# Kernel tuning notes

Measured on AMD Instinct MI355X. Metric: run time of the kernel, lower is better.

## Reference

```python
import jax, jax.numpy as jnp
import numpy as np

N_NODES = 50000
N_EDGES = 800000
IN_CH, HID, OUT_CH = 128, 256, 40


def setup_inputs() -> dict:
    key = jax.random.key(0)
    ks = jax.random.split(key, 10)
    x = jax.random.normal(ks[0], (N_NODES, IN_CH), dtype=jnp.float32)
    edge_index = jax.random.randint(ks[1], (2, N_EDGES), 0, N_NODES, dtype=jnp.int64)
    s = 0.05  # weight init scale
    return {
        "x": x,
        "edge_index": edge_index,
        "W1a": jax.random.normal(ks[2], (IN_CH, HID), dtype=jnp.float32) * s,
        "b1a": jnp.zeros((HID,), jnp.float32),
        "W2a": jax.random.normal(ks[3], (HID, HID), dtype=jnp.float32) * s,
        "b2a": jnp.zeros((HID,), jnp.float32),
        "W1b": jax.random.normal(ks[4], (HID, HID), dtype=jnp.float32) * s,
        "b1b": jnp.zeros((HID,), jnp.float32),
        "W2b": jax.random.normal(ks[5], (HID, HID), dtype=jnp.float32) * s,
        "b2b": jnp.zeros((HID,), jnp.float32),
        "Wlin": jax.random.normal(ks[6], (HID * 2, OUT_CH), dtype=jnp.float32) * s,
        "blin": jnp.zeros((OUT_CH,), jnp.float32),
    }


def _gin_conv(h, src, dst, W1, b1, W2, b2):
    # sum-aggregate messages h[src] into destination nodes, eps = 0
    agg = jax.ops.segment_sum(h[src], dst, num_segments=N_NODES)
    z = h + agg
    z = jnp.maximum(z @ W1 + b1, 0.0) @ W2 + b2  # 2-layer MLP
    return z


def reference(x, edge_index, W1a, b1a, W2a, b2a, W1b, b1b, W2b, b2b, Wlin, blin):
    src, dst = edge_index[0], edge_index[1]
    h1 = jnp.maximum(_gin_conv(x, src, dst, W1a, b1a, W2a, b2a), 0.0)
    h2 = jnp.maximum(_gin_conv(h1, src, dst, W1b, b1b, W2b, b2b), 0.0)
    h_cat = jnp.concatenate([h1, h2], axis=1)  # [N, 2*HID]
    logits = h_cat @ Wlin + blin
    return jax.nn.log_softmax(logits, axis=1)
```

## Files before the change

### kernel.cpp

```cpp
#include <hip/hip_runtime.h>
#include <math.h>

#define N_NODES 50000
#define N_EDGES 800000
#define IN_CH 128
#define HID 256
#define OUT_CH 40
#define GRP 6250
#define HGRP 3125
#define NCHUNK 32
#define TS 264

typedef unsigned short u16;
typedef unsigned char u8;
typedef __attribute__((ext_vector_type(8))) short bf16x8;
typedef __attribute__((ext_vector_type(8))) unsigned short u16x8;
typedef __attribute__((ext_vector_type(4))) float f32x4;
typedef __attribute__((ext_vector_type(2))) float f32x2;

__device__ __forceinline__ float bf2f(u16 u) {
    union { unsigned int i; float f; } v; v.i = ((unsigned int)u) << 16; return v.f;
}
__device__ __forceinline__ u16 f2bf(float f) {
    union { float f; unsigned int i; } v; v.f = f;
    unsigned int x = v.i;
    x += 0x7fffu + ((x >> 16) & 1u);
    return (u16)(x >> 16);
}

#define GLOBAL_AS __attribute__((address_space(1)))
#define LDS_AS __attribute__((address_space(3)))
__device__ __forceinline__ void async_cp16(const void* g, void* l) {
    __builtin_amdgcn_global_load_lds((const GLOBAL_AS unsigned int*)g,
                                     (LDS_AS unsigned int*)l, 16, 0, 0);
}

__device__ __forceinline__ void pack_w(
    const float* __restrict__ in, u16* __restrict__ out, int K, int N, int c)
{
    for (int k = threadIdx.x; k < K; k += 256) {
        int kk32 = k >> 5, quad = (k >> 3) & 3, e = k & 7;
        size_t base = (((size_t)c * (K >> 5) + kk32) * 64 + quad * 16) * 8 + e;
#pragma unroll
        for (int li = 0; li < 16; li++) {
            int n = c * 16 + li;
            float v = (n < N) ? in[(size_t)k * N + n] : 0.f;
            out[base + (size_t)li * 8] = f2bf(v);
        }
    }
}

__global__ __launch_bounds__(256) void prep_fused(
    const float* __restrict__ x, u16* __restrict__ xb, u8* __restrict__ xf8,
    const int* __restrict__ ei, u16* __restrict__ e16,
    const float* __restrict__ W1a, const float* __restrict__ W2a,
    const float* __restrict__ W1b, const float* __restrict__ W2b,
    const float* __restrict__ Wlin,
    u16* __restrict__ W1aPk, u16* __restrict__ W2aPk,
    u16* __restrict__ W1bPk, u16* __restrict__ W2bPk, u16* __restrict__ WlinPk,
    u16* __restrict__ partial)
{
    __shared__ int hist[HGRP];
    int b = blockIdx.x;
    if (b < 6250) {
        int i = b * 256 + threadIdx.x;
        float4 v = ((const float4*)x)[i];
        ushort4 o;
        o.x = f2bf(v.x); o.y = f2bf(v.y); o.z = f2bf(v.z); o.w = f2bf(v.w);
        ((ushort4*)xb)[i] = o;
        int p = __builtin_amdgcn_cvt_pk_fp8_f32(v.x, v.y, 0, false);
        p = __builtin_amdgcn_cvt_pk_fp8_f32(v.z, v.w, p, true);
        ((unsigned int*)xf8)[i] = (unsigned int)p;
    } else if (b < 7813) {
        int i = (b - 6250) * 256 + threadIdx.x;
        if (i < (2 * N_EDGES) / 4) {
            int4 v = ((const int4*)ei)[i];
            ushort4 o;
            o.x = (u16)v.x; o.y = (u16)v.y; o.z = (u16)v.z; o.w = (u16)v.w;
            ((ushort4*)e16)[i] = o;
        }
    } else if (b < 7880) {
        int t = b - 7813;
        if (t < 16)       pack_w(W1a, W1aPk, IN_CH, HID, t);
        else if (t < 32)  pack_w(W2a, W2aPk, HID, HID, t - 16);
        else if (t < 48)  pack_w(W1b, W1bPk, HID, HID, t - 32);
        else if (t < 64)  pack_w(W2b, W2bPk, HID, HID, t - 48);
        else              pack_w(Wlin, WlinPk, 2 * HID, OUT_CH, t - 64);
    } else {
        const int hb = b - 7880;
        const int gh = hb & 15;
        const int sub = hb >> 4;
        const int lo = gh * HGRP;
        const int CH = N_EDGES / NCHUNK;
        for (int i = threadIdx.x; i < HGRP; i += 256) hist[i] = 0;
        __syncthreads();
        const int4* dsts = (const int4*)(ei + N_EDGES + sub * CH);
        for (int k = threadIdx.x; k < CH / 4; k += 256) {
            int4 d = dsts[k];
            int r0 = d.x - lo, r1 = d.y - lo;
            int r2 = d.z - lo, r3 = d.w - lo;
            if ((unsigned)r0 < (unsigned)HGRP) atomicAdd(&hist[r0], 1);
            if ((unsigned)r1 < (unsigned)HGRP) atomicAdd(&hist[r1], 1);
            if ((unsigned)r2 < (unsigned)HGRP) atomicAdd(&hist[r2], 1);
            if ((unsigned)r3 < (unsigned)HGRP) atomicAdd(&hist[r3], 1);
        }
        __syncthreads();
        u16* po = partial + (size_t)(sub * 8 + (gh >> 1)) * GRP + (gh & 1) * HGRP;
        for (int i = threadIdx.x; i < HGRP; i += 256) po[i] = (u16)hist[i];
    }
}

__global__ __launch_bounds__(256) void scan1(
    const u16* __restrict__ partial, u16* __restrict__ chunkpref,
    int* __restrict__ excl, int* __restrict__ partials_out)
{
    __shared__ int lds[256];
    const int tid = threadIdx.x;
    const int node = blockIdx.x * 256 + tid;
    int d = 0;
    if (node < N_NODES) {
        int g = node / GRP;
        int off = node - g * GRP;
#pragma unroll
        for (int sub = 0; sub < NCHUNK; sub++) {
            chunkpref[(size_t)sub * N_NODES + node] = (u16)d;
            d += partial[(size_t)(sub * 8 + g) * GRP + off];
        }
    }
    lds[tid] = d;
    __syncthreads();
    for (int off = 1; off < 256; off <<= 1) {
        int t = (tid >= off) ? lds[tid - off] : 0;
        __syncthreads();
        lds[tid] += t;
        __syncthreads();
    }
    if (node < N_NODES) excl[node] = lds[tid] - d;
    if (tid == 255) partials_out[blockIdx.x] = lds[255];
}

__global__ __launch_bounds__(256) void scan3(
    int* __restrict__ excl, const int* __restrict__ partials,
    int* __restrict__ sentinel, int nPart)
{
    __shared__ int lds[256];
    __shared__ int bp[256];
    const int tid = threadIdx.x;
    int orig = (tid < nPart) ? partials[tid] : 0;
    lds[tid] = orig;
    __syncthreads();
    for (int off = 1; off < 256; off <<= 1) {
        int t = (tid >= off) ? lds[tid - off] : 0;
        __syncthreads();
        lds[tid] += t;
        __syncthreads();
    }
    bp[tid] = lds[tid] - orig;
    __syncthreads();
    const int idx = blockIdx.x * 256 + tid;
    if (idx < N_NODES) excl[idx] += bp[blockIdx.x];
    if (idx == 0) sentinel[0] = N_EDGES;
}

__global__ __launch_bounds__(256) void csr_fill(
    const u16* __restrict__ src16, const u16* __restrict__ dst16,
    const int* __restrict__ rowp, const u16* __restrict__ chunkpref,
    u16* __restrict__ csr_src)
{
    __shared__ int cur[HGRP];
    const int gh = blockIdx.x & 15;
    const int c = blockIdx.x >> 4;
    const int lo = gh * HGRP;
    const int CH = N_EDGES / NCHUNK;
    const u16* cp = chunkpref + (size_t)c * N_NODES + lo;
    for (int i = threadIdx.x; i < HGRP; i += 256)
        cur[i] = rowp[lo + i] + cp[i];
    __syncthreads();
    const ushort4* dsts = (const ushort4*)(dst16 + c * CH);
    const ushort4* srcs = (const ushort4*)(src16 + c * CH);
    for (int k = threadIdx.x; k < CH / 4; k += 256) {
        ushort4 d = dsts[k];
        ushort4 sc = srcs[k];
        int r0 = (int)d.x - lo, r1 = (int)d.y - lo;
        int r2 = (int)d.z - lo, r3 = (int)d.w - lo;
        if ((unsigned)r0 < (unsigned)HGRP) { int p = atomicAdd(&cur[r0], 1); csr_src[p] = sc.x; }
        if ((unsigned)r1 < (unsigned)HGRP) { int p = atomicAdd(&cur[r1], 1); csr_src[p] = sc.y; }
        if ((unsigned)r2 < (unsigned)HGRP) { int p = atomicAdd(&cur[r2], 1); csr_src[p] = sc.z; }
        if ((unsigned)r3 < (unsigned)HGRP) { int p = atomicAdd(&cur[r3], 1); csr_src[p] = sc.w; }
    }
}


__global__ __launch_bounds__(256) void gather_agg_f8_128(
    const u16* __restrict__ feat_bf, const u8* __restrict__ feat_f8,
    const int* __restrict__ row_ptr, const int* __restrict__ row_end,
    const u16* __restrict__ csr_src, u16* __restrict__ out)
{
    const int tid = threadIdx.x;
    const int lane = tid & 63;
    const int wv = tid >> 6;
    const int li = lane & 7;
    int node = blockIdx.x * 32 + wv * 8 + (lane >> 3);
    const bool valid = node < N_NODES;
    if (!valid) node = N_NODES - 1;

    int j = row_ptr[node];
    int deg = valid ? (row_end[node] - j) : 0;

    float acc[16];
    {
        u16x8 s0 = *(const u16x8*)(feat_bf + (size_t)node * IN_CH + li * 16);
        u16x8 s1 = *(const u16x8*)(feat_bf + (size_t)node * IN_CH + li * 16 + 8);
#pragma unroll
        for (int q = 0; q < 8; q++) { acc[q] = bf2f(s0[q]); acc[8 + q] = bf2f(s1[q]); }
    }

    int maxdeg = deg;
#pragma unroll
    for (int off = 8; off < 64; off <<= 1)
        maxdeg = max(maxdeg, __shfl_xor(maxdeg, off, 64));

    for (int it = 0; it < maxdeg; it += 4) {
        int4 g0 = {0,0,0,0}, g1 = {0,0,0,0}, g2 = {0,0,0,0}, g3 = {0,0,0,0};
        if (it < deg)
            g0 = *(const int4*)(feat_f8 + (size_t)csr_src[j + it] * IN_CH + li * 16);
        if (it + 1 < deg)
            g1 = *(const int4*)(feat_f8 + (size_t)csr_src[j + it + 1] * IN_CH + li * 16);
        if (it + 2 < deg)
            g2 = *(const int4*)(feat_f8 + (size_t)csr_src[j + it + 2] * IN_CH + li * 16);
        if (it + 3 < deg)
            g3 = *(const int4*)(feat_f8 + (size_t)csr_src[j + it + 3] * IN_CH + li * 16);
#pragma unroll
        for (int q = 0; q < 4; q++) {
            int w0 = (&g0.x)[q], w1 = (&g1.x)[q], w2 = (&g2.x)[q], w3 = (&g3.x)[q];
            f32x2 l0 = __builtin_amdgcn_cvt_pk_f32_fp8(w0, false);
            f32x2 h0 = __builtin_amdgcn_cvt_pk_f32_fp8(w0, true);
            f32x2 l1 = __builtin_amdgcn_cvt_pk_f32_fp8(w1, false);
            f32x2 h1 = __builtin_amdgcn_cvt_pk_f32_fp8(w1, true);
            f32x2 l2 = __builtin_amdgcn_cvt_pk_f32_fp8(w2, false);
            f32x2 h2 = __builtin_amdgcn_cvt_pk_f32_fp8(w2, true);
            f32x2 l3 = __builtin_amdgcn_cvt_pk_f32_fp8(w3, false);
            f32x2 h3 = __builtin_amdgcn_cvt_pk_f32_fp8(w3, true);
            acc[q * 4 + 0] += (l0.x + l1.x) + (l2.x + l3.x);
            acc[q * 4 + 1] += (l0.y + l1.y) + (l2.y + l3.y);
            acc[q * 4 + 2] += (h0.x + h1.x) + (h2.x + h3.x);
            acc[q * 4 + 3] += (h0.y + h1.y) + (h2.y + h3.y);
        }
    }

    if (valid) {
        u16x8 o0, o1;
#pragma unroll
        for (int q = 0; q < 8; q++) { o0[q] = f2bf(acc[q]); o1[q] = f2bf(acc[8 + q]); }
        *(u16x8*)(out + (size_t)node * IN_CH + li * 16) = o0;
        *(u16x8*)(out + (size_t)node * IN_CH + li * 16 + 8) = o1;
    }
}

__global__ __launch_bounds__(256) void gather_agg_f8_256(
    const u16* __restrict__ feat_bf, const u8* __restrict__ feat_f8,
    const int* __restrict__ row_ptr, const int* __restrict__ row_end,
    const u16* __restrict__ csr_src, u16* __restrict__ out)
{
    const int tid = threadIdx.x;
    const int lane = tid & 63;
    const int wv = tid >> 6;
    const int li = lane & 15;
    const int node = blockIdx.x * 16 + wv * 4 + (lane >> 4);

    int j = row_ptr[node];
    int deg = row_end[node] - j;

    float acc[16];
    {
        u16x8 s0 = *(const u16x8*)(feat_bf + (size_t)node * HID + li * 16);
        u16x8 s1 = *(const u16x8*)(feat_bf + (size_t)node * HID + li * 16 + 8);
#pragma unroll
        for (int q = 0; q < 8; q++) { acc[q] = bf2f(s0[q]); acc[8 + q] = bf2f(s1[q]); }
    }

    int maxdeg = deg;
#pragma unroll
    for (int off = 16; off < 64; off <<= 1)
        maxdeg = max(maxdeg, __shfl_xor(maxdeg, off, 64));

    for (int it = 0; it < maxdeg; it += 4) {
        int4 g0 = {0,0,0,0}, g1 = {0,0,0,0}, g2 = {0,0,0,0}, g3 = {0,0,0,0};
        if (it < deg)
            g0 = *(const int4*)(feat_f8 + (size_t)csr_src[j + it] * HID + li * 16);
        if (it + 1 < deg)
            g1 = *(const int4*)(feat_f8 + (size_t)csr_src[j + it + 1] * HID + li * 16);
        if (it + 2 < deg)
            g2 = *(const int4*)(feat_f8 + (size_t)csr_src[j + it + 2] * HID + li * 16);
        if (it + 3 < deg)
            g3 = *(const int4*)(feat_f8 + (size_t)csr_src[j + it + 3] * HID + li * 16);
#pragma unroll
        for (int q = 0; q < 4; q++) {
            int w0 = (&g0.x)[q], w1 = (&g1.x)[q], w2 = (&g2.x)[q], w3 = (&g3.x)[q];
            f32x2 l0 = __builtin_amdgcn_cvt_pk_f32_fp8(w0, false);
            f32x2 h0 = __builtin_amdgcn_cvt_pk_f32_fp8(w0, true);
            f32x2 l1 = __builtin_amdgcn_cvt_pk_f32_fp8(w1, false);
            f32x2 h1 = __builtin_amdgcn_cvt_pk_f32_fp8(w1, true);
            f32x2 l2 = __builtin_amdgcn_cvt_pk_f32_fp8(w2, false);
            f32x2 h2 = __builtin_amdgcn_cvt_pk_f32_fp8(w2, true);
            f32x2 l3 = __builtin_amdgcn_cvt_pk_f32_fp8(w3, false);
            f32x2 h3 = __builtin_amdgcn_cvt_pk_f32_fp8(w3, true);
            acc[q * 4 + 0] += (l0.x + l1.x) + (l2.x + l3.x);
            acc[q * 4 + 1] += (l0.y + l1.y) + (l2.y + l3.y);
            acc[q * 4 + 2] += (h0.x + h1.x) + (h2.x + h3.x);
            acc[q * 4 + 3] += (h0.y + h1.y) + (h2.y + h3.y);
        }
    }

    u16x8 o0, o1;
#pragma unroll
    for (int q = 0; q < 8; q++) { o0[q] = f2bf(acc[q]); o1[q] = f2bf(acc[8 + q]); }
    *(u16x8*)(out + (size_t)node * HID + li * 16) = o0;
    *(u16x8*)(out + (size_t)node * HID + li * 16 + 8) = o1;
}

__global__ __launch_bounds__(256, 4) void mlp_fused(
    const u16* __restrict__ A, int K1,
    const u16* __restrict__ W1pk, const float* __restrict__ b1,
    const u16* __restrict__ W2pk, const float* __restrict__ b2,
    u16* __restrict__ out, u8* __restrict__ outF8, int M)
{
    __shared__ u16 SB[64 * TS];

    const int tid = threadIdx.x;
    const int lane = tid & 63;
    const int wid = tid >> 6;
    const int li = lane & 15;
    const int quad = lane >> 4;
    const int koff = quad * 8;
    const int row0 = blockIdx.x * 64;
    const int KB1 = K1 >> 5;
    const int rsh = (K1 == 256) ? 9 : 8;

    {
        const u8* Ag = (const u8*)(A + (size_t)row0 * K1);
        const int rounds = K1 >> 5;
        for (int j = 0; j < rounds; j++) {
            int L = (j * 256 + tid) * 16;
            int G = L ^ (((L >> rsh) & 7) << 4);
            async_cp16(Ag + G, (u8*)SB + L);
        }
    }

    f32x4 acc[4][4];
#pragma unroll
    for (int i = 0; i < 4; i++)
#pragma unroll
        for (int j = 0; j < 4; j++) acc[i][j] = (f32x4){0.f, 0.f, 0.f, 0.f};

#define LDW(WF, WPK, KB, KK32)                                                \
    {   _Pragma("unroll")                                                     \
        for (int t = 0; t < 4; t++)                                           \
            WF[t] = *(const bf16x8*)((WPK) +                                  \
                (((size_t)(wid * 4 + t) * (KB) + (KK32)) * 64 + lane) * 8); }
#define LDA1(AF, KK)                                                          \
    {   _Pragma("unroll")                                                     \
        for (int t = 0; t < 4; t++) {                                         \
            int row = t * 16 + li;                                            \
            int bo = row * (K1 * 2) + ((KK) + koff) * 2;                      \
            bo ^= (row & 7) << 4;                                             \
            AF[t] = *(const bf16x8*)((const u8*)SB + bo); } }
#define LDA2(AF, KK)                                                          \
    {   _Pragma("unroll")                                                     \
        for (int t = 0; t < 4; t++)                                           \
            AF[t] = *(const bf16x8*)(SB + (t * 16 + li) * TS + (KK) + koff); }
#define MFMA16(AF, WF)                                                        \
    {   _Pragma("unroll")                                                     \
        for (int mt = 0; mt < 4; mt++)                                        \
            _Pragma("unroll")                                                 \
            for (int nt = 0; nt < 4; nt++)                                    \
                acc[mt][nt] = __builtin_amdgcn_mfma_f32_16x16x32_bf16(        \
                    AF[mt], WF[nt], acc[mt][nt], 0, 0, 0); }

    bf16x8 wfA[4], wfB[4], af[4];

    LDW(wfA, W1pk, KB1, 0);
    __syncthreads();

    for (int kk32 = 0; kk32 < KB1; kk32 += 2) {
        LDW(wfB, W1pk, KB1, kk32 + 1);
        LDA1(af, kk32 * 32);
        MFMA16(af, wfA);
        if (kk32 + 2 < KB1) LDW(wfA, W1pk, KB1, kk32 + 2);
        LDA1(af, kk32 * 32 + 32);
        MFMA16(af, wfB);
    }
    __syncthreads();

#pragma unroll
    for (int nt = 0; nt < 4; nt++) {
        int col = wid * 64 + nt * 16 + li;
        float bv = b1[col];
#pragma unroll
        for (int mt = 0; mt < 4; mt++) {
#pragma unroll
            for (int reg = 0; reg < 4; reg++) {
                int row = mt * 16 + quad * 4 + reg;
                float v = fmaxf(acc[mt][nt][reg] + bv, 0.f);
                SB[row * TS + col] = f2bf(v);
                acc[mt][nt][reg] = 0.f;
            }
        }
    }
    LDW(wfA, W2pk, 8, 0);
    __syncthreads();

    for (int kk32 = 0; kk32 < 8; kk32 += 2) {
        LDW(wfB, W2pk, 8, kk32 + 1);
        LDA2(af, kk32 * 32);
        MFMA16(af, wfA);
        if (kk32 + 2 < 8) LDW(wfA, W2pk, 8, kk32 + 2);
        LDA2(af, kk32 * 32 + 32);
        MFMA16(af, wfB);
    }
#undef LDW
#undef LDA1
#undef LDA2
#undef MFMA16

    __syncthreads();
#pragma unroll
    for (int nt = 0; nt < 4; nt++) {
        int col = wid * 64 + nt * 16 + li;
        float bv = b2[col];
#pragma unroll
        for (int mt = 0; mt < 4; mt++) {
#pragma unroll
            for (int reg = 0; reg < 4; reg++) {
                int row = mt * 16 + quad * 4 + reg;
                float v = fmaxf(acc[mt][nt][reg] + bv, 0.f);
                SB[row * TS + col] = f2bf(v);
            }
        }
    }
    __syncthreads();
#pragma unroll
    for (int it = 0; it < 8; it++) {
        int flat = it * 4096 + tid * 16;
        int r = flat >> 9;
        int cu = (flat & 511) >> 1;
        int row = row0 + r;
        if (row < M) {
            u16x8 v = *(const u16x8*)(SB + r * TS + cu);
            *(u16x8*)(out + (size_t)row * HID + cu) = v;
            if (outF8 != nullptr) {
                int p0 = __builtin_amdgcn_cvt_pk_fp8_f32(bf2f(v[0]), bf2f(v[1]), 0, false);
                p0 = __builtin_amdgcn_cvt_pk_fp8_f32(bf2f(v[2]), bf2f(v[3]), p0, true);
                int p1 = __builtin_amdgcn_cvt_pk_fp8_f32(bf2f(v[4]), bf2f(v[5]), 0, false);
                p1 = __builtin_amdgcn_cvt_pk_fp8_f32(bf2f(v[6]), bf2f(v[7]), p1, true);
                int2 pv; pv.x = p0; pv.y = p1;
                *(int2*)(outF8 + (size_t)row * HID + cu) = pv;
            }
        }
    }
}

__global__ __launch_bounds__(256, 6) void gemm_mfma(
    const u16* __restrict__ A, const u16* __restrict__ Acat, int Ksplit, int ldA,
    const u16* __restrict__ Bpk, const float* __restrict__ bias,
    float* __restrict__ out, int M, int K)
{
    const int tid = threadIdx.x;
    const int lane = tid & 63;
    const int wid = tid >> 6;
    const int li = lane & 15;
    const int quad = lane >> 4;
    const int koff = quad * 8;
    const int row0 = blockIdx.x * 64 + wid * 16;

    f32x4 acc[3];
#pragma unroll
    for (int i = 0; i < 3; i++) acc[i] = (f32x4){0.f, 0.f, 0.f, 0.f};

    int r = row0 + li;
    const int arow = (r < M) ? r : (M - 1);
    const int KB = K >> 5;

#define LD_G(AF, BF, KK)                                                      \
    {   const u16* Ab = ((KK) >= Ksplit) ? Acat : A;                          \
        const int kb = ((KK) >= Ksplit) ? ((KK) - Ksplit) : (KK);             \
        AF = *(const bf16x8*)(Ab + (size_t)arow * ldA + kb + koff);           \
        _Pragma("unroll")                                                     \
        for (int t = 0; t < 3; t++)                                           \
            BF[t] = *(const bf16x8*)(Bpk +                                    \
                (((size_t)t * KB + ((KK) >> 5)) * 64 + lane) * 8); }
#define MFMA3(AF, BF)                                                         \
    {   _Pragma("unroll")                                                     \
        for (int nt = 0; nt < 3; nt++)                                        \
            acc[nt] = __builtin_amdgcn_mfma_f32_16x16x32_bf16(                \
                AF, BF[nt], acc[nt], 0, 0, 0); }

    {
        bf16x8 a0, b0[3], a1, b1v[3];
        LD_G(a0, b0, 0);
        for (int kk = 0; kk < K; kk += 64) {
            LD_G(a1, b1v, kk + 32);
            MFMA3(a0, b0);
            if (kk + 64 < K) LD_G(a0, b0, kk + 64);
            MFMA3(a1, b1v);
        }
    }
#undef LD_G
#undef MFMA3

    float b0v = bias[li];
    float b1s = bias[16 + li];
    float b2s = (li < 8) ? bias[32 + li] : 0.f;
#pragma unroll
    for (int reg = 0; reg < 4; reg++) {
        int row = row0 + quad * 4 + reg;
        float v0 = acc[0][reg] + b0v;
        float v1 = acc[1][reg] + b1s;
        float v2 = (li < 8) ? (acc[2][reg] + b2s) : -INFINITY;
        float m = fmaxf(fmaxf(v0, v1), v2);
#pragma unroll
        for (int off = 1; off < 16; off <<= 1)
            m = fmaxf(m, __shfl_xor(m, off, 64));
        float s = expf(v0 - m) + expf(v1 - m)
                + ((li < 8) ? expf(v2 - m) : 0.f);
#pragma unroll
        for (int off = 1; off < 16; off <<= 1)
            s += __shfl_xor(s, off, 64);
        float lg = m + logf(s);
        if (row < M) {
            out[(size_t)row * OUT_CH + li] = v0 - lg;
            out[(size_t)row * OUT_CH + 16 + li] = v1 - lg;
            if (li < 8) out[(size_t)row * OUT_CH + 32 + li] = v2 - lg;
        }
    }
}

extern "C" void kernel_launch(void* const* d_in, const int* in_sizes, int n_in,
                              void* d_out, int out_size, void* d_ws, size_t ws_size,
                              hipStream_t stream)
{
    const float* x    = (const float*)d_in[0];
    const int*   ei   = (const int*)d_in[1];
    const float* W1a  = (const float*)d_in[2];
    const float* b1a  = (const float*)d_in[3];
    const float* W2a  = (const float*)d_in[4];
    const float* b2a  = (const float*)d_in[5];
    const float* W1b  = (const float*)d_in[6];
    const float* b1b  = (const float*)d_in[7];
    const float* W2b  = (const float*)d_in[8];
    const float* b2b  = (const float*)d_in[9];
    const float* Wlin = (const float*)d_in[10];
    const float* blin = (const float*)d_in[11];
    float* out = (float*)d_out;

    const size_t R = (size_t)N_NODES * HID;
    u16* R0 = (u16*)d_ws;
    u16* R1 = R0 + R;
    u16* R2 = R1 + R;
    u16* R3 = R2 + R;
    u16* R4 = R3 + R;
    u16* xbf = R0;
    u16* zA  = R1;
    u16* partial = (u16*)R1;
    u8*  xf8 = (u8*)(R1 + (size_t)N_NODES * IN_CH);
    u8*  h1f8 = (u8*)R1;
    u16* h1  = R3;
    u16* zB  = R4;
    u16* h2  = R2;

    u16* wts = R4 + R;
    u16* W1aPk = wts;
    u16* W2aPk = W1aPk + 256 * 128;
    u16* W1bPk = W2aPk + 256 * 256;
    u16* W2bPk = W1bPk + 256 * 256;
    u16* WlinPk = W2bPk + 256 * 256;
    int* rowp   = (int*)(WlinPk + 128 * 512);
    int* part   = rowp + N_NODES + 64;
    u16* csr    = (u16*)(part + 256);
    u16* e16    = csr + N_EDGES;
    u16* src16  = e16;
    u16* dst16  = e16 + N_EDGES;
    u16* chunkpref = dst16 + N_EDGES;

    dim3 blk(256);
    const int scanBlocks = (N_NODES + 255) / 256;
    const int agg128Blocks = (N_NODES + 31) / 32;
    const int agg256Blocks = N_NODES / 16;
    const int mlpBlocks  = (N_NODES + 63) / 64;
    const int gemmBlocks = (N_NODES + 63) / 64;

    prep_fused<<<8392, blk, 0, stream>>>(x, xbf, xf8, ei, e16,
                                         W1a, W2a, W1b, W2b, Wlin,
                                         W1aPk, W2aPk, W1bPk, W2bPk, WlinPk,
                                         partial);
    scan1<<<scanBlocks, blk, 0, stream>>>(partial, chunkpref, rowp, part);
    scan3<<<scanBlocks, blk, 0, stream>>>(rowp, part, rowp + N_NODES, scanBlocks);
    csr_fill<<<16 * NCHUNK, blk, 0, stream>>>(src16, dst16, rowp, chunkpref, csr);

    gather_agg_f8_128<<<agg128Blocks, blk, 0, stream>>>(xbf, xf8, rowp, rowp + 1, csr, zA);
    mlp_fused<<<mlpBlocks, blk, 0, stream>>>(zA, IN_CH, W1aPk, b1a, W2aPk, b2a,
                                             h1, h1f8, N_NODES);

    gather_agg_f8_256<<<agg256Blocks, blk, 0, stream>>>(h1, h1f8, rowp, rowp + 1, csr, zB);
    mlp_fused<<<mlpBlocks, blk, 0, stream>>>(zB, HID, W1bPk, b1b, W2bPk, b2b,
                                             h2, nullptr, N_NODES);

    gemm_mfma<<<gemmBlocks, blk, 0, stream>>>(h1, h2, HID, HID, WlinPk, blin,
                                              out, N_NODES, 2 * HID);
}
```

Baseline: 252.1 us.

## Swizzle MLP shared tile and stage final GEMM A rows through LDS

The fused MLP kernel drops its padded shared-memory row stride (264) for an unpadded 256-wide tile with an XOR swizzle. This shrinks LDS per block so occupancy can rise from 4 to 5 blocks. The final linear+log_softmax GEMM now copies each 64-row tile of h1 and then h2 into a swizzled LDS buffer with async copies before running the MFMAs, where it previously loaded A fragments straight from global memory. The goal is coalesced global reads; the cost is extra LDS usage, extra barriers and occupancy lowered from 6 to 5 in the GEMM. The GEMM tail no longer clamps rows past M, so the last block may read past the end of h1/h2.

```diff
diff --git a/kernel.cpp b/kernel.cpp
--- a/kernel.cpp
+++ b/kernel.cpp
@@ -9,7 +9,6 @@
 #define GRP 6250
 #define HGRP 3125
 #define NCHUNK 32
-#define TS 264
 
 typedef unsigned short u16;
 typedef unsigned char u8;
@@ -319,13 +318,13 @@
     *(u16x8*)(out + (size_t)node * HID + li * 16 + 8) = o1;
 }
 
-__global__ __launch_bounds__(256, 4) void mlp_fused(
+__global__ __launch_bounds__(256, 5) void mlp_fused(
     const u16* __restrict__ A, int K1,
     const u16* __restrict__ W1pk, const float* __restrict__ b1,
     const u16* __restrict__ W2pk, const float* __restrict__ b2,
     u16* __restrict__ out, u8* __restrict__ outF8, int M)
 {
-    __shared__ u16 SB[64 * TS];
+    __shared__ u16 SB[64 * 256];
 
     const int tid = threadIdx.x;
     const int lane = tid & 63;
@@ -367,8 +366,10 @@
             AF[t] = *(const bf16x8*)((const u8*)SB + bo); } }
 #define LDA2(AF, KK)                                                          \
     {   _Pragma("unroll")                                                     \
-        for (int t = 0; t < 4; t++)                                           \
-            AF[t] = *(const bf16x8*)(SB + (t * 16 + li) * TS + (KK) + koff); }
+        for (int t = 0; t < 4; t++) {                                         \
+            int row = t * 16 + li;                                            \
+            int ix = (row * 256 + (KK) + koff) ^ ((row & 7) << 3);            \
+            AF[t] = *(const bf16x8*)(SB + ix); } }
 #define MFMA16(AF, WF)                                                        \
     {   _Pragma("unroll")                                                     \
         for (int mt = 0; mt < 4; mt++)                                        \
@@ -402,7 +403,7 @@
             for (int reg = 0; reg < 4; reg++) {
                 int row = mt * 16 + quad * 4 + reg;
                 float v = fmaxf(acc[mt][nt][reg] + bv, 0.f);
-                SB[row * TS + col] = f2bf(v);
+                SB[(row * 256 + col) ^ ((row & 7) << 3)] = f2bf(v);
                 acc[mt][nt][reg] = 0.f;
             }
         }
@@ -434,7 +435,7 @@
             for (int reg = 0; reg < 4; reg++) {
                 int row = mt * 16 + quad * 4 + reg;
                 float v = fmaxf(acc[mt][nt][reg] + bv, 0.f);
-                SB[row * TS + col] = f2bf(v);
+                SB[(row * 256 + col) ^ ((row & 7) << 3)] = f2bf(v);
             }
         }
     }
@@ -446,7 +447,8 @@
         int cu = (flat & 511) >> 1;
         int row = row0 + r;
         if (row < M) {
-            u16x8 v = *(const u16x8*)(SB + r * TS + cu);
+            int ix = (r * 256 + cu) ^ ((r & 7) << 3);
+            u16x8 v = *(const u16x8*)(SB + ix);
             *(u16x8*)(out + (size_t)row * HID + cu) = v;
             if (outF8 != nullptr) {
                 int p0 = __builtin_amdgcn_cvt_pk_fp8_f32(bf2f(v[0]), bf2f(v[1]), 0, false);
@@ -460,52 +462,76 @@
     }
 }
 
-__global__ __launch_bounds__(256, 6) void gemm_mfma(
-    const u16* __restrict__ A, const u16* __restrict__ Acat, int Ksplit, int ldA,
+__global__ __launch_bounds__(256, 5) void gemm_mfma(
+    const u16* __restrict__ A, const u16* __restrict__ Acat,
     const u16* __restrict__ Bpk, const float* __restrict__ bias,
-    float* __restrict__ out, int M, int K)
-{
+    float* __restrict__ out, int M)
+{
+    __shared__ u16 SA[64 * 256];
+
     const int tid = threadIdx.x;
     const int lane = tid & 63;
     const int wid = tid >> 6;
     const int li = lane & 15;
     const int quad = lane >> 4;
     const int koff = quad * 8;
-    const int row0 = blockIdx.x * 64 + wid * 16;
+    const int row0 = blockIdx.x * 64;
+    const int rloc = wid * 16 + li;
 
     f32x4 acc[3];
 #pragma unroll
     for (int i = 0; i < 3; i++) acc[i] = (f32x4){0.f, 0.f, 0.f, 0.f};
 
-    int r = row0 + li;
-    const int arow = (r < M) ? r : (M - 1);
-    const int KB = K >> 5;
-
-#define LD_G(AF, BF, KK)                                                      \
-    {   const u16* Ab = ((KK) >= Ksplit) ? Acat : A;                          \
-        const int kb = ((KK) >= Ksplit) ? ((KK) - Ksplit) : (KK);             \
-        AF = *(const bf16x8*)(Ab + (size_t)arow * ldA + kb + koff);           \
+#define STAGE(SRC)                                                            \
+    {   const u8* Ag = (const u8*)((SRC) + (size_t)row0 * 256);               \
         _Pragma("unroll")                                                     \
+        for (int j = 0; j < 8; j++) {                                         \
+            int L = (j * 256 + tid) * 16;                                     \
+            int G = L ^ (((L >> 9) & 7) << 4);                                \
+            async_cp16(Ag + G, (u8*)SA + L); } }
+#define LDA_S(AF, KB32)                                                       \
+    {   int bo = rloc * 512 + ((KB32) * 32 + koff) * 2;                       \
+        bo ^= (rloc & 7) << 4;                                                \
+        AF = *(const bf16x8*)((const u8*)SA + bo); }
+#define LDB_S(BF, KK32)                                                       \
+    {   _Pragma("unroll")                                                     \
         for (int t = 0; t < 3; t++)                                           \
             BF[t] = *(const bf16x8*)(Bpk +                                    \
-                (((size_t)t * KB + ((KK) >> 5)) * 64 + lane) * 8); }
+                (((size_t)t * 16 + (KK32)) * 64 + lane) * 8); }
 #define MFMA3(AF, BF)                                                         \
     {   _Pragma("unroll")                                                     \
         for (int nt = 0; nt < 3; nt++)                                        \
             acc[nt] = __builtin_amdgcn_mfma_f32_16x16x32_bf16(                \
                 AF, BF[nt], acc[nt], 0, 0, 0); }
 
-    {
-        bf16x8 a0, b0[3], a1, b1v[3];
-        LD_G(a0, b0, 0);
-        for (int kk = 0; kk < K; kk += 64) {
-            LD_G(a1, b1v, kk + 32);
-            MFMA3(a0, b0);
-            if (kk + 64 < K) LD_G(a0, b0, kk + 64);
-            MFMA3(a1, b1v);
-        }
-    }
-#undef LD_G
+    bf16x8 a0, b0[3], a1, b1v[3];
+
+    STAGE(A);
+    LDB_S(b0, 0);
+    __syncthreads();
+    for (int k = 0; k < 8; k += 2) {
+        LDB_S(b1v, k + 1);
+        LDA_S(a0, k);
+        MFMA3(a0, b0);
+        if (k + 2 < 8) LDB_S(b0, k + 2);
+        LDA_S(a1, k + 1);
+        MFMA3(a1, b1v);
+    }
+    __syncthreads();
+    STAGE(Acat);
+    LDB_S(b0, 8);
+    __syncthreads();
+    for (int k = 8; k < 16; k += 2) {
+        LDB_S(b1v, k + 1);
+        LDA_S(a0, k - 8);
+        MFMA3(a0, b0);
+        if (k + 2 < 16) LDB_S(b0, k + 2);
+        LDA_S(a1, k - 7);
+        MFMA3(a1, b1v);
+    }
+#undef STAGE
+#undef LDA_S
+#undef LDB_S
 #undef MFMA3
 
     float b0v = bias[li];
@@ -513,7 +539,7 @@
     float b2s = (li < 8) ? bias[32 + li] : 0.f;
 #pragma unroll
     for (int reg = 0; reg < 4; reg++) {
-        int row = row0 + quad * 4 + reg;
+        int row = row0 + wid * 16 + quad * 4 + reg;
         float v0 = acc[0][reg] + b0v;
         float v1 = acc[1][reg] + b1s;
         float v2 = (li < 8) ? (acc[2][reg] + b2s) : -INFINITY;
@@ -605,6 +631,5 @@
     mlp_fused<<<mlpBlocks, blk, 0, stream>>>(zB, HID, W1bPk, b1b, W2bPk, b2b,
                                              h2, nullptr, N_NODES);
 
-    gemm_mfma<<<gemmBlocks, blk, 0, stream>>>(h1, h2, HID, HID, WlinPk, blin,
-                                              out, N_NODES, 2 * HID);
-}
+    gemm_mfma<<<gemmBlocks, blk, 0, stream>>>(h1, h2, WlinPk, blin, out, N_NODES);
+}
```

Result: slower. 416.1 us (+65.1%).
